# Kernel tuning notes

Hardware: AMD Instinct MI355X
Metric: run time of the kernel (lower is better)

Reference implementation:

```python
import jax, jax.numpy as jnp
import numpy as np

D_MODEL = 256; D_FFN = 1024; N_HEADS = 8; N_LEVELS = 4
N_FRAMES = 6; T_WIN = 5  # enc_connect_all_embeddings: attend to all T-1 other frames
N_CUR = 4; N_TMP = 2; P_TOT = N_CUR + T_WIN * N_TMP  # 14 points per (head, level)
SHAPES = np.array([[6, 48, 64], [6, 24, 32], [6, 12, 16], [6, 6, 8]], dtype=np.int64)  # (T,H,W) per level


def _lin(k, dout, din):
    s = 1.0 / np.sqrt(din)
    kw, kb = jax.random.split(k)
    return (jax.random.uniform(kw, (dout, din), jnp.float32, -s, s),
            jax.random.uniform(kb, (dout,), jnp.float32, -s, s))


def setup_inputs() -> dict:
    key = jax.random.key(0)
    ks = jax.random.split(key, 16)
    sizes = SHAPES[:, 0] * SHAPES[:, 1] * SHAPES[:, 2]
    Lq = int(sizes.sum())
    lsi = np.concatenate([[0], np.cumsum(sizes)[:-1]])
    inp = {
        'src': jax.random.normal(ks[0], (1, Lq, D_MODEL), jnp.float32),
        'pos': 0.1 * jax.random.normal(ks[1], (1, Lq, D_MODEL), jnp.float32),
        'spatial_shapes': jnp.asarray(SHAPES),
        'level_start_index': jnp.asarray(lsi),
        'valid_ratios': jnp.ones((1, N_LEVELS, 2), jnp.float32),
    }
    names = ['W_samp', 'W_tsamp', 'W_attn', 'W_val', 'W_out', 'W_ff1', 'W_ff2']
    douts = [N_HEADS * N_LEVELS * N_CUR * 2, N_HEADS * N_LEVELS * T_WIN * N_TMP * 2,
             N_HEADS * N_LEVELS * P_TOT, D_MODEL, D_MODEL, D_FFN, D_MODEL]
    dins = [D_MODEL, D_MODEL, D_MODEL, D_MODEL, D_MODEL, D_MODEL, D_FFN]
    for i, (n, do, di) in enumerate(zip(names, douts, dins)):
        w, b = _lin(ks[2 + i], do, di)
        inp[n] = w
        inp[n.replace('W_', 'b_')] = b
    inp['norm1_g'] = jnp.ones((D_MODEL,), jnp.float32); inp['norm1_b'] = jnp.zeros((D_MODEL,), jnp.float32)
    inp['norm2_g'] = jnp.ones((D_MODEL,), jnp.float32); inp['norm2_b'] = jnp.zeros((D_MODEL,), jnp.float32)
    return inp


def _ln(x, g, b, eps=1e-5):
    m = x.mean(-1, keepdims=True)
    v = jnp.mean((x - m) ** 2, -1, keepdims=True)
    return (x - m) * jax.lax.rsqrt(v + eps) * g + b


def _ref_and_toffs(shapes, valid_ratios):
    # Mirrors get_reference_points + generate_temporal_offsets_all_connect (vectorized per level).
    refs, toffs = [], []
    for l in range(shapes.shape[0]):
        T, H, W = (int(shapes[l, 0]), int(shapes[l, 1]), int(shapes[l, 2]))
        ry, rx = jnp.meshgrid(jnp.linspace(0.5, H * T - 0.5, H * T, dtype=jnp.float32),
                              jnp.linspace(0.5, W - 0.5, W, dtype=jnp.float32), indexing='ij')
        ry = ry.reshape(-1) / (valid_ratios[0, l, 1] * H * T)
        rx = rx.reshape(-1) / (valid_ratios[0, l, 0] * W)
        refs.append(jnp.stack((rx, ry), -1))
        j = np.arange(T)
        mat = (j[None, :] - j[:, None]).astype(np.float32) / T  # (target - curr)/T
        offd = mat[~np.eye(T, dtype=bool)].reshape(T, T - 1)    # drop t==0
        val = jnp.repeat(jnp.asarray(offd), H * W, axis=0)      # frame-major, matches flatten order
        toffs.append(jnp.stack([jnp.zeros_like(val), val], -1))
    ref = jnp.concatenate(refs, 0)[None]                     # [1,Lq,2]
    ref = ref[:, :, None] * valid_ratios[0][None, None]      # [1,Lq,L,2]
    to = jnp.concatenate(toffs, 0)                           # [Lq,T-1,2]
    to = to[:, None] * valid_ratios[0][None, :, None]        # [Lq,L,T-1,2]
    return ref, to


def _msdeform(value, shapes, lsi, loc, attn):
    # value [N,Len,nH,Dh]; loc [N,Lq,nH,L,P,2] in [0,1]; attn [N,Lq,nH,L,P]
    N, _, nH, Dh = value.shape
    out = 0.0
    for l in range(shapes.shape[0]):
        T, H, W = (int(shapes[l, 0]), int(shapes[l, 1]), int(shapes[l, 2]))
        Ht = T * H; s = int(lsi[l])
        v = value[:, s:s + Ht * W].transpose(0, 2, 1, 3)  # [N,nH,S,Dh]
        x = loc[:, :, :, l, :, 0] * W - 0.5   # grid_sample align_corners=False
        y = loc[:, :, :, l, :, 1] * Ht - 0.5
        x0 = jnp.floor(x); y0 = jnp.floor(y)
        fx = x - x0; fy = y - y0
        acc = 0.0
        for dy in (0, 1):
            for dx in (0, 1):
                xi = x0 + dx; yi = y0 + dy
                w = (fx if dx else 1.0 - fx) * (fy if dy else 1.0 - fy)
                w = w * ((xi >= 0) & (xi < W) & (yi >= 0) & (yi < Ht))  # zero padding
                idx = (jnp.clip(yi, 0, Ht - 1) * W + jnp.clip(xi, 0, W - 1)).astype(jnp.int32)
                idx = idx.transpose(0, 2, 1, 3)  # [N,nH,Lq,P]
                g = jax.vmap(jax.vmap(lambda vv, ii: vv[ii]))(v, idx)  # [N,nH,Lq,P,Dh]
                acc = acc + g * w.transpose(0, 2, 1, 3)[..., None]
        out = out + jnp.einsum('nhqpd,nqhp->nqhd', acc, attn[:, :, :, l])
    return out  # [N,Lq,nH,Dh]


def reference(src, pos, spatial_shapes, level_start_index, valid_ratios,
              W_samp, b_samp, W_tsamp, b_tsamp, W_attn, b_attn, W_val, b_val,
              W_out, b_out, W_ff1, b_ff1, W_ff2, b_ff2,
              norm1_g, norm1_b, norm2_g, norm2_b):
    shapes = np.asarray(spatial_shapes); lsi = np.asarray(level_start_index)
    N, Lq, _ = src.shape
    ref, to = _ref_and_toffs(shapes, valid_ratios)
    norm = jnp.asarray(np.stack([shapes[:, 2], shapes[:, 0] * shapes[:, 1]], -1), jnp.float32)  # [L,2]=(W,H*T)
    q = src + pos  # with_pos_embed
    value = (src @ W_val.T + b_val).reshape(N, Lq, N_HEADS, D_MODEL // N_HEADS)
    samp = (q @ W_samp.T + b_samp).reshape(N, Lq, N_HEADS, N_LEVELS, N_CUR, 2)
    tsamp = (q @ W_tsamp.T + b_tsamp).reshape(N, Lq, N_HEADS, N_LEVELS, T_WIN, N_TMP, 2)
    aw = jax.nn.softmax((q @ W_attn.T + b_attn).reshape(N, Lq, N_HEADS, N_LEVELS * P_TOT), -1)
    aw = aw.reshape(N, Lq, N_HEADS, N_LEVELS, P_TOT)
    loc_cur = ref[:, :, None, :, None, :] + samp / norm[None, None, None, :, None, :]
    base_t = ref[:, :, None, :, None, :] + to[None, :, None, :, :, :]            # [1,Lq,1,L,tw,2]
    loc_tmp = base_t[:, :, :, :, :, None, :] + tsamp / norm[None, None, None, :, None, None, :]
    loc_tmp = loc_tmp.reshape(N, Lq, N_HEADS, N_LEVELS, T_WIN * N_TMP, 2)
    loc = jnp.concatenate([loc_cur, loc_tmp], axis=4)  # [N,Lq,nH,L,P_TOT,2]
    o = _msdeform(value, shapes, lsi, loc, aw).reshape(N, Lq, D_MODEL)
    src2 = o @ W_out.T + b_out
    x = _ln(src + src2, norm1_g, norm1_b)
    ff = jax.nn.relu(x @ W_ff1.T + b_ff1) @ W_ff2.T + b_ff2
    return _ln(x + ff, norm2_g, norm2_b)
```

## Files before the change

kernel.cpp:

```cpp
#include <hip/hip_runtime.h>
#include <hip/hip_bf16.h>
#include <hip/hip_fp16.h>
#include <math.h>

#define LQ 24480
#define QSTRIDE 1408

typedef short bf16x8 __attribute__((ext_vector_type(8)));
typedef float f32x4 __attribute__((ext_vector_type(4)));
typedef float f32x4v __attribute__((ext_vector_type(4)));

static __device__ __forceinline__ float bf2f(ushort u) {
    union { unsigned int i; float f; } v; v.i = ((unsigned int)u) << 16; return v.f;
}
static __device__ __forceinline__ ushort f2bf(float f) {
    __hip_bfloat16 h = __float2bfloat16(f);
    return *reinterpret_cast<ushort*>(&h);
}
static __device__ __forceinline__ ushort f2h(float f) {
    __half h = __float2half(f);
    return *reinterpret_cast<ushort*>(&h);
}
static __device__ __forceinline__ float u2f_lo(unsigned int u) {
    union { unsigned int i; float f; } v; v.i = u << 16; return v.f;
}
static __device__ __forceinline__ float u2f_hi(unsigned int u) {
    union { unsigned int i; float f; } v; v.i = u & 0xffff0000u; return v.f;
}
static __device__ __forceinline__ void pkf16_lo(unsigned& acc, unsigned v, unsigned w) {
    asm("v_pk_fma_f16 %0, %1, %2, %0 op_sel:[0,0,0] op_sel_hi:[1,0,1]"
        : "+v"(acc) : "v"(v), "v"(w));
}
static __device__ __forceinline__ void pkf16_hi(unsigned& acc, unsigned v, unsigned w) {
    asm("v_pk_fma_f16 %0, %1, %2, %0 op_sel:[0,1,0] op_sel_hi:[1,1,1]"
        : "+v"(acc) : "v"(v), "v"(w));
}

template <int RELU, int F16OUT>
static __device__ __forceinline__ void gemm_lds128(
    const ushort* __restrict__ A, const ushort* __restrict__ W,
    const float* __restrict__ bias, ushort* __restrict__ Cb,
    int M, int N, int K, int bm, int bn,
    ushort* As, ushort* Bs, int tid)
{
    const int wave = tid >> 6, lane = tid & 63;
    const int wm = wave >> 1, wn = wave & 1;
    const int r = lane & 15, kblk4 = lane >> 4;

    const int skb = tid & 3;
    const int sr0 = tid >> 2;
    const ushort* gA0 = A + (size_t)min(bm + sr0,      M - 1) * K + skb * 8;
    const ushort* gA1 = A + (size_t)min(bm + 64 + sr0, M - 1) * K + skb * 8;
    const ushort* gB0 = W + (size_t)(bn + sr0) * K + skb * 8;
    const ushort* gB1 = W + (size_t)(bn + 64 + sr0) * K + skb * 8;
    const int wA0 = skb * 1032 + sr0 * 8;
    const int wA1 = skb * 1032 + (64 + sr0) * 8;
    const int wB0 = skb * 1032 + ((sr0 & 3) * 32 + (sr0 >> 2)) * 8;
    const int wB1 = skb * 1032 + (((64 + sr0) & 3) * 32 + ((64 + sr0) >> 2)) * 8;

    f32x4 acc[4][4] = {};

    bf16x8 ga0 = *(const bf16x8*)gA0;
    bf16x8 ga1 = *(const bf16x8*)gA1;
    bf16x8 gb0 = *(const bf16x8*)gB0;
    bf16x8 gb1 = *(const bf16x8*)gB1;
    *(bf16x8*)(As + wA0) = ga0;
    *(bf16x8*)(As + wA1) = ga1;
    *(bf16x8*)(Bs + wB0) = gb0;
    *(bf16x8*)(Bs + wB1) = gb1;

    const int NK = K >> 5;
    int buf = 0;
    for (int kt = 0; kt < NK; ++kt) {
        __syncthreads();
        if (kt + 1 < NK) {
            int ko = (kt + 1) * 32;
            ga0 = *(const bf16x8*)(gA0 + ko);
            ga1 = *(const bf16x8*)(gA1 + ko);
            gb0 = *(const bf16x8*)(gB0 + ko);
            gb1 = *(const bf16x8*)(gB1 + ko);
        }
        const ushort* Ab = As + buf * 4128;
        const ushort* Bb = Bs + buf * 4128;
        bf16x8 a[4], b[4];
#pragma unroll
        for (int i = 0; i < 4; ++i)
            a[i] = *(const bf16x8*)(Ab + kblk4 * 1032 + (wm * 64 + i * 16 + r) * 8);
#pragma unroll
        for (int j = 0; j < 4; ++j)
            b[j] = *(const bf16x8*)(Bb + kblk4 * 1032 + (j * 32 + wn * 16 + r) * 8);
#pragma unroll
        for (int i = 0; i < 4; ++i)
#pragma unroll
            for (int j = 0; j < 4; ++j)
                acc[i][j] = __builtin_amdgcn_mfma_f32_16x16x32_bf16(a[i], b[j], acc[i][j], 0, 0, 0);
        if (kt + 1 < NK) {
            ushort* An = As + (buf ^ 1) * 4128;
            ushort* Bn = Bs + (buf ^ 1) * 4128;
            *(bf16x8*)(An + wA0) = ga0;
            *(bf16x8*)(An + wA1) = ga1;
            *(bf16x8*)(Bn + wB0) = gb0;
            *(bf16x8*)(Bn + wB1) = gb1;
        }
        buf ^= 1;
    }

    const int c0 = bn + wn * 64 + r * 4;
    if (c0 >= N) return;
    const float4 bv = *(const float4*)(bias + c0);
    const int orow = kblk4 * 4;
#pragma unroll
    for (int i = 0; i < 4; ++i)
#pragma unroll
        for (int t = 0; t < 4; ++t) {
            int rr = bm + wm * 64 + i * 16 + orow + t;
            if (rr < M) {
                float v0 = acc[i][0][t] + bv.x;
                float v1 = acc[i][1][t] + bv.y;
                float v2 = acc[i][2][t] + bv.z;
                float v3 = acc[i][3][t] + bv.w;
                if (RELU) {
                    v0 = fmaxf(v0, 0.f); v1 = fmaxf(v1, 0.f);
                    v2 = fmaxf(v2, 0.f); v3 = fmaxf(v3, 0.f);
                }
                uint2 pk;
                if (F16OUT) {
                    pk.x = (unsigned)f2h(v0) | ((unsigned)f2h(v1) << 16);
                    pk.y = (unsigned)f2h(v2) | ((unsigned)f2h(v3) << 16);
                } else {
                    pk.x = (unsigned)f2bf(v0) | ((unsigned)f2bf(v1) << 16);
                    pk.y = (unsigned)f2bf(v2) | ((unsigned)f2bf(v3) << 16);
                }
                *(uint2*)(Cb + (size_t)rr * N + c0) = pk;
            }
        }
}

__global__ __launch_bounds__(256) void gemm_valq(
    const ushort* __restrict__ srcb, const ushort* __restrict__ qb,
    const ushort* __restrict__ Wv, const ushort* __restrict__ Wq,
    const float* __restrict__ b_val, const float* __restrict__ bq,
    ushort* __restrict__ valh, ushort* __restrict__ qout)
{
    __shared__ ushort As[2 * 4128];
    __shared__ ushort Bs[2 * 4128];
    const int bx = blockIdx.x;
    if (bx < 2) {
        gemm_lds128<0, 1>(srcb, Wv, b_val, valh, LQ, 256, 256,
                          blockIdx.y * 128, bx * 128, As, Bs, threadIdx.x);
    } else {
        gemm_lds128<0, 0>(qb, Wq, bq, qout, LQ, QSTRIDE, 256,
                          blockIdx.y * 128, (bx - 2) * 128, As, Bs, threadIdx.x);
    }
}

__global__ __launch_bounds__(256) void gemm_ff1(
    const ushort* __restrict__ A, const ushort* __restrict__ W,
    const float* __restrict__ bias, ushort* __restrict__ Cb)
{
    __shared__ ushort As[2 * 4128];
    __shared__ ushort Bs[2 * 4128];
    gemm_lds128<1, 0>(A, W, bias, Cb, LQ, 1024, 256,
                      blockIdx.y * 128, blockIdx.x * 128, As, Bs, threadIdx.x);
}

template <int RES16, int WF32, int WBF16>
__global__ __launch_bounds__(256) void gemm_ln(
    const ushort* __restrict__ A, const ushort* __restrict__ W,
    const float* __restrict__ bias, const void* __restrict__ res,
    const float* __restrict__ g, const float* __restrict__ be,
    float* __restrict__ outF, ushort* __restrict__ outB,
    int M, int K)
{
    const int wave = threadIdx.x >> 6;
    const int lane = threadIdx.x & 63;
    const int r = lane & 15;
    const int kblk = lane >> 4;
    const int bm = blockIdx.x * 128;
    const int c0 = r * 16;

    f32x4 acc[2][16] = {};

    int row0 = bm + wave * 32 + r;
    int row1 = row0 + 16;
    row0 = min(row0, M - 1);
    row1 = min(row1, M - 1);
    const ushort* ap0 = A + (size_t)row0 * K + kblk * 8;
    const ushort* ap1 = A + (size_t)row1 * K + kblk * 8;
    const ushort* wp  = W + (size_t)c0 * K + kblk * 8;

#pragma unroll 2
    for (int k = 0; k < K; k += 32) {
        bf16x8 a0 = *(const bf16x8*)(ap0 + k);
        bf16x8 a1 = *(const bf16x8*)(ap1 + k);
#pragma unroll
        for (int ni = 0; ni < 16; ++ni) {
            bf16x8 b = *(const bf16x8*)(wp + (size_t)ni * K + k);
            acc[0][ni] = __builtin_amdgcn_mfma_f32_16x16x32_bf16(a0, b, acc[0][ni], 0, 0, 0);
            acc[1][ni] = __builtin_amdgcn_mfma_f32_16x16x32_bf16(a1, b, acc[1][ni], 0, 0, 0);
        }
    }

    const int orow = kblk * 4;

    float bv[16];
#pragma unroll
    for (int q = 0; q < 4; ++q)
        *(float4*)(bv + q * 4) = *(const float4*)(bias + c0 + q * 4);

    float mean_[2][4], rstd_[2][4];
#pragma unroll
    for (int mi = 0; mi < 2; ++mi)
#pragma unroll
        for (int j = 0; j < 4; ++j) {
            int rr = bm + wave * 32 + mi * 16 + orow + j;
            int rl = min(rr, M - 1);
            float rv[16];
            if (RES16) {
                const ushort* r16 = (const ushort*)res + (size_t)rl * 256 + c0;
                uint4 ra = *(const uint4*)r16;
                uint4 rb = *(const uint4*)(r16 + 8);
                unsigned ru[8] = {ra.x, ra.y, ra.z, ra.w, rb.x, rb.y, rb.z, rb.w};
#pragma unroll
                for (int b = 0; b < 8; ++b) {
                    rv[2 * b]     = u2f_lo(ru[b]);
                    rv[2 * b + 1] = u2f_hi(ru[b]);
                }
            } else {
                const float* rp = (const float*)res + (size_t)rl * 256 + c0;
#pragma unroll
                for (int q = 0; q < 4; ++q)
                    *(float4*)(rv + q * 4) = *(const float4*)(rp + q * 4);
            }
            float s = 0.f, s2 = 0.f;
#pragma unroll
            for (int ni = 0; ni < 16; ++ni) {
                float v = acc[mi][ni][j] + bv[ni] + rv[ni];
                acc[mi][ni][j] = v;
                s += v; s2 += v * v;
            }
#pragma unroll
            for (int off = 8; off; off >>= 1) {
                s  += __shfl_xor(s,  off, 16);
                s2 += __shfl_xor(s2, off, 16);
            }
            float mu = s * (1.f / 256.f);
            float var = s2 * (1.f / 256.f) - mu * mu;
            mean_[mi][j] = mu;
            rstd_[mi][j] = rsqrtf(var + 1e-5f);
        }

    float gv[16], bev[16];
#pragma unroll
    for (int q = 0; q < 4; ++q) {
        *(float4*)(gv + q * 4)  = *(const float4*)(g + c0 + q * 4);
        *(float4*)(bev + q * 4) = *(const float4*)(be + c0 + q * 4);
    }

#pragma unroll
    for (int mi = 0; mi < 2; ++mi)
#pragma unroll
        for (int j = 0; j < 4; ++j) {
            int rr = bm + wave * 32 + mi * 16 + orow + j;
            if (rr < M) {
                float o[16];
#pragma unroll
                for (int ni = 0; ni < 16; ++ni)
                    o[ni] = (acc[mi][ni][j] - mean_[mi][j]) * rstd_[mi][j] * gv[ni] + bev[ni];
                if (WF32) {
#pragma unroll
                    for (int q = 0; q < 4; ++q)
                        *(float4*)(outF + (size_t)rr * 256 + c0 + q * 4) = *(float4*)(o + q * 4);
                }
                if (WBF16) {
                    uint pk[8];
#pragma unroll
                    for (int b = 0; b < 8; ++b)
                        pk[b] = (unsigned)f2bf(o[2 * b]) | ((unsigned)f2bf(o[2 * b + 1]) << 16);
                    *(uint4*)(outB + (size_t)rr * 256 + c0)     = *(uint4*)pk;
                    *(uint4*)(outB + (size_t)rr * 256 + c0 + 8) = *(uint4*)(pk + 4);
                }
            }
        }
}

struct CvtArgs {
    const float* s[10]; void* d[10]; int n[10]; int isbf[10]; int bcnt[10];
    const float* src; const float* pos; ushort* srcb; ushort* qb;
    int nsrc4; int bsrc;
};
__global__ __launch_bounds__(256) void cvt_all(CvtArgs a)
{
    int b = blockIdx.x;
    if (b < a.bsrc) {
        int i = b * 256 + threadIdx.x;
        if (i >= a.nsrc4) return;
        f32x4v s = *(const f32x4v*)(a.src + (size_t)i * 4);
        f32x4v p = *(const f32x4v*)(a.pos + (size_t)i * 4);
        ushort us[4], uq[4];
#pragma unroll
        for (int j = 0; j < 4; ++j) { us[j] = f2bf(s[j]); uq[j] = f2bf(s[j] + p[j]); }
        *(ulong1*)(a.srcb + (size_t)i * 4) = *(ulong1*)us;
        *(ulong1*)(a.qb   + (size_t)i * 4) = *(ulong1*)uq;
        return;
    }
    b -= a.bsrc;
    int seg = 0;
    while (seg < 9 && b >= a.bcnt[seg]) { b -= a.bcnt[seg]; ++seg; }
    int i = b * 256 + threadIdx.x;
    if (i >= a.n[seg]) return;
    float v = a.s[seg][i];
    if (a.isbf[seg]) ((ushort*)a.d[seg])[i] = f2bf(v);
    else             ((float*)a.d[seg])[i]  = v;
}

__global__ __launch_bounds__(256) void deform_kernel(
    const ushort* __restrict__ valh,
    const ushort* __restrict__ qout,
    const float* __restrict__ vr,
    ushort* __restrict__ ob)
{
    const int q0 = blockIdx.x * 2;
    const int tid = threadIdx.x;

    __shared__ int4  offs_s[2][448];
    __shared__ uint2 wts_s[2][448];

    const int lsiA[4] = {0, 18432, 23040, 24192};

    {
        int grp = tid >> 4;
        int ql = grp >> 3, h = grp & 7;
        int ln = tid & 15;
        const ushort* lg = qout + (size_t)(q0 + ql) * QSTRIDE + 896 + h * 56;
        float l0 = bf2f(lg[ln]);
        float l1 = bf2f(lg[16 + ln]);
        float l2 = bf2f(lg[32 + ln]);
        float l3 = (ln < 8) ? bf2f(lg[48 + ln]) : -1e30f;
        float m = fmaxf(fmaxf(l0, l1), fmaxf(l2, l3));
#pragma unroll
        for (int off = 8; off; off >>= 1) m = fmaxf(m, __shfl_xor(m, off, 16));
        float e0 = expf(l0 - m), e1 = expf(l1 - m), e2 = expf(l2 - m);
        float e3 = (ln < 8) ? expf(l3 - m) : 0.f;
        float s = e0 + e1 + e2 + e3;
#pragma unroll
        for (int off = 8; off; off >>= 1) s += __shfl_xor(s, off, 16);
        float inv = 1.f / s;
        *(float*)&wts_s[ql][h * 56 + ln]      = e0 * inv;
        *(float*)&wts_s[ql][h * 56 + 16 + ln] = e1 * inv;
        *(float*)&wts_s[ql][h * 56 + 32 + ln] = e2 * inv;
        if (ln < 8) *(float*)&wts_s[ql][h * 56 + 48 + ln] = e3 * inv;
    }

    int lqv = (q0 >= 24192) ? 3 : (q0 >= 23040) ? 2 : (q0 >= 18432) ? 1 : 0;
    int Wqv = 64 >> lqv, Hqv = 48 >> lqv;
    int slq = lsiA[lqv];
    float vrxq = vr[2 * lqv], vryq = vr[2 * lqv + 1];
    float rxb0, ryb0, rxb1, ryb1; int tq0, tq1;
    {
        int qi = q0 - slq;
        int iy = qi >> (6 - lqv);
        int jx = qi & (Wqv - 1);
        tq0 = iy / Hqv;
        rxb0 = ((float)jx + 0.5f) / (vrxq * (float)Wqv);
        ryb0 = ((float)iy + 0.5f) / (vryq * (float)(Hqv * 6));
        qi += 1;
        iy = qi >> (6 - lqv);
        jx = qi & (Wqv - 1);
        tq1 = iy / Hqv;
        rxb1 = ((float)jx + 0.5f) / (vrxq * (float)Wqv);
        ryb1 = ((float)iy + 0.5f) / (vryq * (float)(Hqv * 6));
    }
    __syncthreads();

    for (int it = tid; it < 896; it += 256) {
        int ql = (it >= 448) ? 1 : 0;
        int item = it - ql * 448;
        float rx_base = ql ? rxb1 : rxb0;
        float ry_base = ql ? ryb1 : ryb0;
        int tq = ql ? tq1 : tq0;

        int h = item / 56;
        int p = item - h * 56;
        int l = p / 14;
        int pp = p - l * 14;

        int Wl = 64 >> l;
        int Hl = 48 >> l;
        int Htl = Hl * 6;
        float vrx = vr[2 * l], vry = vr[2 * l + 1];

        float aw = *(const float*)&wts_s[ql][item];

        const ushort* qrow = qout + (size_t)(q0 + ql) * QSTRIDE;
        float ox, oy, ty;
        if (pp < 4) {
            ox = bf2f(qrow[h * 32 + l * 8 + pp * 2]);
            oy = bf2f(qrow[h * 32 + l * 8 + pp * 2 + 1]);
            ty = 0.f;
        } else {
            int pq = pp - 4;
            int tw = pq >> 1, nt = pq & 1;
            int tt = (tw < tq) ? tw : tw + 1;
            ty = (float)(tt - tq) * vry * (float)Hl;
            ox = bf2f(qrow[256 + h * 80 + l * 20 + tw * 4 + nt * 2]);
            oy = bf2f(qrow[256 + h * 80 + l * 20 + tw * 4 + nt * 2 + 1]);
        }
        float x = rx_base * vrx * (float)Wl - 0.5f + ox;
        float y = ry_base * vry * (float)Htl - 0.5f + ty + oy;
        float x0f = floorf(x), y0f = floorf(y);
        int x0 = (int)x0f, y0 = (int)y0f;
        float fx = x - x0f, fy = y - y0f;

        int xi0 = min(max(x0, 0), Wl - 1);
        int xi1 = min(max(x0 + 1, 0), Wl - 1);
        int yi0 = min(max(y0, 0), Htl - 1);
        int yi1 = min(max(y0 + 1, 0), Htl - 1);
        float mx0 = (x0 >= 0 && x0 < Wl) ? 1.f : 0.f;
        float mx1 = (x0 >= -1 && x0 + 1 < Wl) ? 1.f : 0.f;
        float my0 = (y0 >= 0 && y0 < Htl) ? 1.f : 0.f;
        float my1 = (y0 >= -1 && y0 + 1 < Htl) ? 1.f : 0.f;

        float gx0 = (1.f - fx) * mx0;
        float gx1 = fx * mx1;
        float gy0 = (1.f - fy) * my0 * aw;
        float gy1 = fy * my1 * aw;

        int sl = lsiA[l];
        int rb0 = (sl + yi0 * Wl) * 512;
        int rb1 = (sl + yi1 * Wl) * 512;
        offs_s[ql][item] = make_int4(rb0 + xi0 * 512, rb0 + xi1 * 512,
                                     rb1 + xi0 * 512, rb1 + xi1 * 512);
        __half2 hA = __halves2half2(__float2half(gy0 * gx0), __float2half(gy0 * gx1));
        __half2 hB = __halves2half2(__float2half(gy1 * gx0), __float2half(gy1 * gx1));
        wts_s[ql][item] = make_uint2(*(const unsigned*)&hA, *(const unsigned*)&hB);
    }
    __syncthreads();

    const int ql = tid >> 7;
    const int h = (tid >> 4) & 7;
    const int c2 = tid & 15;
    const unsigned laneByte = (unsigned)(h * 64 + c2 * 4);
    const char* vbase = (const char*)valh;
    const int4* op = offs_s[ql] + h * 56;
    const uint2* wp = wts_s[ql] + h * 56;
    unsigned acc = 0;
#pragma unroll 8
    for (int p = 0; p < 56; ++p) {
        int4 o4 = op[p];
        uint2 w2 = wp[p];
        unsigned u0 = *(const unsigned*)(vbase + (size_t)(unsigned)(o4.x + laneByte));
        unsigned u1 = *(const unsigned*)(vbase + (size_t)(unsigned)(o4.y + laneByte));
        unsigned u2 = *(const unsigned*)(vbase + (size_t)(unsigned)(o4.z + laneByte));
        unsigned u3 = *(const unsigned*)(vbase + (size_t)(unsigned)(o4.w + laneByte));
        pkf16_lo(acc, u0, w2.x);
        pkf16_hi(acc, u1, w2.x);
        pkf16_lo(acc, u2, w2.y);
        pkf16_hi(acc, u3, w2.y);
    }
    float2 af = __half22float2(*(const __half2*)&acc);
    unsigned packed = (unsigned)f2bf(af.x) | ((unsigned)f2bf(af.y) << 16);
    *(unsigned*)(ob + (size_t)(q0 + ql) * 256 + h * 32 + c2 * 2) = packed;
}

extern "C" void kernel_launch(void* const* d_in, const int* in_sizes, int n_in,
                              void* d_out, int out_size, void* d_ws, size_t ws_size,
                              hipStream_t stream)
{
    const float* src    = (const float*)d_in[0];
    const float* pos    = (const float*)d_in[1];
    const float* vr     = (const float*)d_in[4];
    const float* W_samp = (const float*)d_in[5];
    const float* b_samp = (const float*)d_in[6];
    const float* W_tsamp= (const float*)d_in[7];
    const float* b_tsamp= (const float*)d_in[8];
    const float* W_attn = (const float*)d_in[9];
    const float* b_attn = (const float*)d_in[10];
    const float* W_val  = (const float*)d_in[11];
    const float* b_val  = (const float*)d_in[12];
    const float* W_out  = (const float*)d_in[13];
    const float* b_out  = (const float*)d_in[14];
    const float* W_ff1  = (const float*)d_in[15];
    const float* b_ff1  = (const float*)d_in[16];
    const float* W_ff2  = (const float*)d_in[17];
    const float* b_ff2  = (const float*)d_in[18];
    const float* n1g    = (const float*)d_in[19];
    const float* n1b    = (const float*)d_in[20];
    const float* n2g    = (const float*)d_in[21];
    const float* n2b    = (const float*)d_in[22];

    float* ws = (float*)d_ws;
    ushort* qout  = (ushort*)ws;
    float* valueR = ws + (size_t)LQ * 704;
    ushort* valh  = (ushort*)valueR;
    ushort* srcb  = (ushort*)(valueR + (size_t)LQ * 256);
    ushort* qb    = srcb + (size_t)LQ * 256;
    ushort* obuf  = qb + (size_t)LQ * 256;
    float* ffB    = (float*)(obuf + (size_t)LQ * 256);
    ushort* Wq    = (ushort*)(ffB + (size_t)LQ * 256);
    ushort* Wv    = Wq + 1408 * 256;
    ushort* Wo    = Wv + 256 * 256;
    ushort* Wf1   = Wo + 256 * 256;
    ushort* Wf2   = Wf1 + 1024 * 256;
    float* bq     = (float*)(Wf2 + 1024 * 256);
    ushort* xB16  = (ushort*)qout;
    ushort* hB16  = (ushort*)valueR;

    CvtArgs ca;
    ca.s[0] = W_samp;  ca.d[0] = Wq;             ca.n[0] = 256 * 256;  ca.isbf[0] = 1;
    ca.s[1] = W_tsamp; ca.d[1] = Wq + 256 * 256; ca.n[1] = 640 * 256;  ca.isbf[1] = 1;
    ca.s[2] = W_attn;  ca.d[2] = Wq + 896 * 256; ca.n[2] = 448 * 256;  ca.isbf[2] = 1;
    ca.s[3] = W_val;   ca.d[3] = Wv;             ca.n[3] = 256 * 256;  ca.isbf[3] = 1;
    ca.s[4] = W_out;   ca.d[4] = Wo;             ca.n[4] = 256 * 256;  ca.isbf[4] = 1;
    ca.s[5] = W_ff1;   ca.d[5] = Wf1;            ca.n[5] = 1024 * 256; ca.isbf[5] = 1;
    ca.s[6] = W_ff2;   ca.d[6] = Wf2;            ca.n[6] = 256 * 1024; ca.isbf[6] = 1;
    ca.s[7] = b_samp;  ca.d[7] = bq;             ca.n[7] = 256;        ca.isbf[7] = 0;
    ca.s[8] = b_tsamp; ca.d[8] = bq + 256;       ca.n[8] = 640;        ca.isbf[8] = 0;
    ca.s[9] = b_attn;  ca.d[9] = bq + 896;       ca.n[9] = 448;        ca.isbf[9] = 0;
    ca.src = src; ca.pos = pos; ca.srcb = srcb; ca.qb = qb;
    ca.nsrc4 = LQ * 64;
    ca.bsrc = (ca.nsrc4 + 255) / 256;
    int total_blocks = ca.bsrc;
    for (int sgi = 0; sgi < 10; ++sgi) {
        ca.bcnt[sgi] = (ca.n[sgi] + 255) / 256;
        total_blocks += ca.bcnt[sgi];
    }
    cvt_all<<<total_blocks, 256, 0, stream>>>(ca);

    const int GM = (LQ + 127) / 128;

    gemm_valq<<<dim3(13, GM), 256, 0, stream>>>(srcb, qb, Wv, Wq, b_val, bq, valh, qout);

    deform_kernel<<<LQ / 2, 256, 0, stream>>>(valh, qout, vr, obuf);

    gemm_ln<0, 0, 1><<<GM, 256, 0, stream>>>(obuf, Wo, b_out, src, n1g, n1b,
                                             nullptr, xB16, LQ, 256);

    gemm_ff1<<<dim3(8, GM), 256, 0, stream>>>(xB16, Wf1, b_ff1, hB16);
    gemm_ln<1, 1, 0><<<GM, 256, 0, stream>>>(hB16, Wf2, b_ff2, xB16, n2g, n2b,
                                             (float*)d_out, nullptr, LQ, 1024);
}
```

Baseline: 325.1 us.

## Stage GEMM tiles with direct global-to-LDS loads instead of register staging

The shared 128x128 bf16 GEMM now fills its double-buffered LDS tiles with global_load_lds instead of loading into registers and then writing to LDS. This removes the LDS write instructions and the register pressure of holding the prefetched tile across the MFMA loop. To fit the per-wave contiguous destination that these loads require, the LDS layout changes from a padded layout to an unpadded one. The B rows are permuted so the fragment reads still index correctly. Two risks come with it: the unpadded layout may cause LDS bank conflicts, and the row clamp on A is gone, so the partial last M tile reads past the end of the input buffer.

```diff
diff --git a/kernel.cpp b/kernel.cpp
--- a/kernel.cpp
+++ b/kernel.cpp
@@ -34,6 +34,12 @@
 static __device__ __forceinline__ void pkf16_hi(unsigned& acc, unsigned v, unsigned w) {
     asm("v_pk_fma_f16 %0, %1, %2, %0 op_sel:[0,1,0] op_sel_hi:[1,1,1]"
         : "+v"(acc) : "v"(v), "v"(w));
+}
+static __device__ __forceinline__ void gload16(const ushort* g, ushort* l) {
+    __builtin_amdgcn_global_load_lds(
+        (const __attribute__((address_space(1))) void*)g,
+        (__attribute__((address_space(3))) void*)l,
+        16, 0, 0);
 }
 
 template <int RELU, int F16OUT>
@@ -43,31 +49,23 @@
     int M, int N, int K, int bm, int bn,
     ushort* As, ushort* Bs, int tid)
 {
-    const int wave = tid >> 6, lane = tid & 63;
-    const int wm = wave >> 1, wn = wave & 1;
+    const int w = tid >> 6, lane = tid & 63;
+    const int wm = w >> 1, wn = w & 1;
     const int r = lane & 15, kblk4 = lane >> 4;
 
-    const int skb = tid & 3;
-    const int sr0 = tid >> 2;
-    const ushort* gA0 = A + (size_t)min(bm + sr0,      M - 1) * K + skb * 8;
-    const ushort* gA1 = A + (size_t)min(bm + 64 + sr0, M - 1) * K + skb * 8;
-    const ushort* gB0 = W + (size_t)(bn + sr0) * K + skb * 8;
-    const ushort* gB1 = W + (size_t)(bn + 64 + sr0) * K + skb * 8;
-    const int wA0 = skb * 1032 + sr0 * 8;
-    const int wA1 = skb * 1032 + (64 + sr0) * 8;
-    const int wB0 = skb * 1032 + ((sr0 & 3) * 32 + (sr0 >> 2)) * 8;
-    const int wB1 = skb * 1032 + (((64 + sr0) & 3) * 32 + ((64 + sr0) >> 2)) * 8;
+    const ushort* gA0 = A + (size_t)(bm + lane) * K + w * 8;
+    const ushort* gA1 = A + (size_t)(bm + 64 + lane) * K + w * 8;
+    const int cB0 = ((lane & 31) << 2) | (lane >> 5);
+    const int cB1 = (((64 + lane) & 31) << 2) | ((64 + lane) >> 5);
+    const ushort* gB0 = W + (size_t)(bn + cB0) * K + w * 8;
+    const ushort* gB1 = W + (size_t)(bn + cB1) * K + w * 8;
+    ushort* lA0 = As + w * 1024;  ushort* lA1 = lA0 + 512;
+    ushort* lB0 = Bs + w * 1024;  ushort* lB1 = lB0 + 512;
 
     f32x4 acc[4][4] = {};
 
-    bf16x8 ga0 = *(const bf16x8*)gA0;
-    bf16x8 ga1 = *(const bf16x8*)gA1;
-    bf16x8 gb0 = *(const bf16x8*)gB0;
-    bf16x8 gb1 = *(const bf16x8*)gB1;
-    *(bf16x8*)(As + wA0) = ga0;
-    *(bf16x8*)(As + wA1) = ga1;
-    *(bf16x8*)(Bs + wB0) = gb0;
-    *(bf16x8*)(Bs + wB1) = gb1;
+    gload16(gA0, lA0); gload16(gA1, lA1);
+    gload16(gB0, lB0); gload16(gB1, lB1);
 
     const int NK = K >> 5;
     int buf = 0;
@@ -75,33 +73,24 @@
         __syncthreads();
         if (kt + 1 < NK) {
             int ko = (kt + 1) * 32;
-            ga0 = *(const bf16x8*)(gA0 + ko);
-            ga1 = *(const bf16x8*)(gA1 + ko);
-            gb0 = *(const bf16x8*)(gB0 + ko);
-            gb1 = *(const bf16x8*)(gB1 + ko);
+            int bo = (buf ^ 1) * 4096;
+            gload16(gA0 + ko, lA0 + bo); gload16(gA1 + ko, lA1 + bo);
+            gload16(gB0 + ko, lB0 + bo); gload16(gB1 + ko, lB1 + bo);
         }
-        const ushort* Ab = As + buf * 4128;
-        const ushort* Bb = Bs + buf * 4128;
+        const ushort* Ab = As + buf * 4096;
+        const ushort* Bb = Bs + buf * 4096;
         bf16x8 a[4], b[4];
 #pragma unroll
         for (int i = 0; i < 4; ++i)
-            a[i] = *(const bf16x8*)(Ab + kblk4 * 1032 + (wm * 64 + i * 16 + r) * 8);
+            a[i] = *(const bf16x8*)(Ab + (kblk4 * 128 + wm * 64 + i * 16 + r) * 8);
 #pragma unroll
         for (int j = 0; j < 4; ++j)
-            b[j] = *(const bf16x8*)(Bb + kblk4 * 1032 + (j * 32 + wn * 16 + r) * 8);
+            b[j] = *(const bf16x8*)(Bb + (kblk4 * 128 + j * 32 + wn * 16 + r) * 8);
 #pragma unroll
         for (int i = 0; i < 4; ++i)
 #pragma unroll
             for (int j = 0; j < 4; ++j)
                 acc[i][j] = __builtin_amdgcn_mfma_f32_16x16x32_bf16(a[i], b[j], acc[i][j], 0, 0, 0);
-        if (kt + 1 < NK) {
-            ushort* An = As + (buf ^ 1) * 4128;
-            ushort* Bn = Bs + (buf ^ 1) * 4128;
-            *(bf16x8*)(An + wA0) = ga0;
-            *(bf16x8*)(An + wA1) = ga1;
-            *(bf16x8*)(Bn + wB0) = gb0;
-            *(bf16x8*)(Bn + wB1) = gb1;
-        }
         buf ^= 1;
     }
 
@@ -142,8 +131,8 @@
     const float* __restrict__ b_val, const float* __restrict__ bq,
     ushort* __restrict__ valh, ushort* __restrict__ qout)
 {
-    __shared__ ushort As[2 * 4128];
-    __shared__ ushort Bs[2 * 4128];
+    __shared__ ushort As[2 * 4096];
+    __shared__ ushort Bs[2 * 4096];
     const int bx = blockIdx.x;
     if (bx < 2) {
         gemm_lds128<0, 1>(srcb, Wv, b_val, valh, LQ, 256, 256,
@@ -158,8 +147,8 @@
     const ushort* __restrict__ A, const ushort* __restrict__ W,
     const float* __restrict__ bias, ushort* __restrict__ Cb)
 {
-    __shared__ ushort As[2 * 4128];
-    __shared__ ushort Bs[2 * 4128];
+    __shared__ ushort As[2 * 4096];
+    __shared__ ushort Bs[2 * 4096];
     gemm_lds128<1, 0>(A, W, bias, Cb, LQ, 1024, 256,
                       blockIdx.y * 128, blockIdx.x * 128, As, Bs, threadIdx.x);
 }
```

Result: slower. 340.2 us (+4.6%).

## Stage gemm_ln operand tiles through double-buffered LDS instead of direct global loads

Applied to the files above, without the earlier changes.

The fused GEMM+LayerNorm kernel used to have each wave load A rows and all 256 weight columns straight from global memory every k-step, so the weight tile was re-read by every wave. It now cooperatively loads 128x32 A and 256x32 B tiles into double-buffered shared memory, with a column permutation on B, and prefetches the next tile into registers while the MFMAs run. This cuts redundant global and L2 traffic but adds about 48KB of LDS per block and a barrier per k-step, which may lower occupancy.

```diff
diff --git a/kernel.cpp b/kernel.cpp
--- a/kernel.cpp
+++ b/kernel.cpp
@@ -172,36 +172,75 @@
     float* __restrict__ outF, ushort* __restrict__ outB,
     int M, int K)
 {
-    const int wave = threadIdx.x >> 6;
-    const int lane = threadIdx.x & 63;
+    __shared__ ushort As[2 * 4128];
+    __shared__ ushort Bs[2 * 8224];
+    const int tid = threadIdx.x;
+    const int wave = tid >> 6;
+    const int lane = tid & 63;
     const int r = lane & 15;
-    const int kblk = lane >> 4;
+    const int kblk4 = lane >> 4;
     const int bm = blockIdx.x * 128;
     const int c0 = r * 16;
 
+    const int skb = tid & 3;
+    const int sr0 = tid >> 2;
+    const ushort* gA0 = A + (size_t)min(bm + sr0,      M - 1) * K + skb * 8;
+    const ushort* gA1 = A + (size_t)min(bm + 64 + sr0, M - 1) * K + skb * 8;
+    const int wA0 = skb * 1032 + sr0 * 8;
+    const int wA1 = skb * 1032 + (64 + sr0) * 8;
+    const ushort* gBp[4]; int wBp[4];
+#pragma unroll
+    for (int i = 0; i < 4; ++i) {
+        int cc = sr0 + 64 * i;
+        gBp[i] = W + (size_t)cc * K + skb * 8;
+        wBp[i] = skb * 2056 + ((((cc) & 15) << 4) | ((cc) >> 4)) * 8;
+    }
+
     f32x4 acc[2][16] = {};
 
-    int row0 = bm + wave * 32 + r;
-    int row1 = row0 + 16;
-    row0 = min(row0, M - 1);
-    row1 = min(row1, M - 1);
-    const ushort* ap0 = A + (size_t)row0 * K + kblk * 8;
-    const ushort* ap1 = A + (size_t)row1 * K + kblk * 8;
-    const ushort* wp  = W + (size_t)c0 * K + kblk * 8;
-
-#pragma unroll 2
-    for (int k = 0; k < K; k += 32) {
-        bf16x8 a0 = *(const bf16x8*)(ap0 + k);
-        bf16x8 a1 = *(const bf16x8*)(ap1 + k);
+    bf16x8 ga0 = *(const bf16x8*)gA0;
+    bf16x8 ga1 = *(const bf16x8*)gA1;
+    bf16x8 gb[4];
+#pragma unroll
+    for (int i = 0; i < 4; ++i) gb[i] = *(const bf16x8*)gBp[i];
+    *(bf16x8*)(As + wA0) = ga0;
+    *(bf16x8*)(As + wA1) = ga1;
+#pragma unroll
+    for (int i = 0; i < 4; ++i) *(bf16x8*)(Bs + wBp[i]) = gb[i];
+
+    const int NK = K >> 5;
+    int buf = 0;
+    for (int kt = 0; kt < NK; ++kt) {
+        __syncthreads();
+        if (kt + 1 < NK) {
+            int ko = (kt + 1) * 32;
+            ga0 = *(const bf16x8*)(gA0 + ko);
+            ga1 = *(const bf16x8*)(gA1 + ko);
+#pragma unroll
+            for (int i = 0; i < 4; ++i) gb[i] = *(const bf16x8*)(gBp[i] + ko);
+        }
+        const ushort* Ab = As + buf * 4128;
+        const ushort* Bb = Bs + buf * 8224;
+        bf16x8 a0 = *(const bf16x8*)(Ab + kblk4 * 1032 + (wave * 32 + r) * 8);
+        bf16x8 a1 = *(const bf16x8*)(Ab + kblk4 * 1032 + (wave * 32 + 16 + r) * 8);
 #pragma unroll
         for (int ni = 0; ni < 16; ++ni) {
-            bf16x8 b = *(const bf16x8*)(wp + (size_t)ni * K + k);
+            bf16x8 b = *(const bf16x8*)(Bb + kblk4 * 2056 + (ni * 16 + r) * 8);
             acc[0][ni] = __builtin_amdgcn_mfma_f32_16x16x32_bf16(a0, b, acc[0][ni], 0, 0, 0);
             acc[1][ni] = __builtin_amdgcn_mfma_f32_16x16x32_bf16(a1, b, acc[1][ni], 0, 0, 0);
         }
-    }
-
-    const int orow = kblk * 4;
+        if (kt + 1 < NK) {
+            ushort* An = As + (buf ^ 1) * 4128;
+            ushort* Bn = Bs + (buf ^ 1) * 8224;
+            *(bf16x8*)(An + wA0) = ga0;
+            *(bf16x8*)(An + wA1) = ga1;
+#pragma unroll
+            for (int i = 0; i < 4; ++i) *(bf16x8*)(Bn + wBp[i]) = gb[i];
+        }
+        buf ^= 1;
+    }
+
+    const int orow = kblk4 * 4;
 
     float bv[16];
 #pragma unroll
```

Result: faster. 278.9 us, median of 2 (-14.2%).
